# Kernel optimization log

Measured on AMD Instinct MI355X. Metric: run time of the kernel, lower is better.

Reference implementation:

```python
import jax, jax.numpy as jnp
import numpy as np
import math

N_EMBD = 1024
N_HEAD = 16
HEAD_DIM = N_EMBD // N_HEAD // 2  # 32
DEPTH = 1
LAMBDA_INIT = 0.8 - 0.6 * math.exp(-0.3 * (DEPTH - 1))  # 0.2
EPS = 1e-5


def setup_inputs() -> dict:
    key = jax.random.key(0)
    ks = jax.random.split(key, 8)
    B, T, C = 4, 1024, N_EMBD
    x = jax.random.normal(ks[0], (B, T, C), dtype=jnp.float32)
    w_attn = jax.random.normal(ks[1], (C, 3 * C), dtype=jnp.float32) * (1.0 / math.sqrt(C))
    w_proj = jax.random.normal(ks[2], (C, C), dtype=jnp.float32) * (1.0 / math.sqrt(C))
    lambda_q1 = jax.random.normal(ks[3], (HEAD_DIM,), dtype=jnp.float32) * 0.1
    lambda_q2 = jax.random.normal(ks[4], (HEAD_DIM,), dtype=jnp.float32) * 0.1
    lambda_k1 = jax.random.normal(ks[5], (HEAD_DIM,), dtype=jnp.float32) * 0.1
    lambda_k2 = jax.random.normal(ks[6], (HEAD_DIM,), dtype=jnp.float32) * 0.1
    gamma = jnp.ones((2 * HEAD_DIM,), dtype=jnp.float32)  # RMSNorm affine weight
    return {"x": x, "w_attn": w_attn, "w_proj": w_proj,
            "lambda_q1": lambda_q1, "lambda_q2": lambda_q2,
            "lambda_k1": lambda_k1, "lambda_k2": lambda_k2, "gamma": gamma}


def reference(x, w_attn, w_proj, lambda_q1, lambda_q2, lambda_k1, lambda_k2, gamma):
    B, T, C = x.shape
    H, hd = N_HEAD, HEAD_DIM
    qkv = x @ w_attn                                  # [B,T,3C]
    q, k, v = jnp.split(qkv, 3, axis=-1)
    q = q.reshape(B, T, 2 * H, hd).transpose(0, 2, 1, 3)   # [B,2H,T,hd]
    k = k.reshape(B, T, 2 * H, hd).transpose(0, 2, 1, 3)   # [B,2H,T,hd]
    v = v.reshape(B, T, H, 2 * hd).transpose(0, 2, 1, 3)   # [B,H,T,2hd]
    q = q * (hd ** -0.5)
    att = jnp.einsum('bhtd,bhsd->bhts', q, k) * (1.0 / math.sqrt(hd))
    causal = jnp.tril(jnp.ones((T, T), dtype=bool))
    att = jnp.where(causal, att, -jnp.inf)
    att = jax.nn.softmax(att, axis=-1)                # [B,2H,T,T]
    lam1 = jnp.exp(jnp.sum(lambda_q1 * lambda_k1))
    lam2 = jnp.exp(jnp.sum(lambda_q2 * lambda_k2))
    lambda_full = lam1 - lam2 + LAMBDA_INIT
    att = att.reshape(B, H, 2, T, T)
    att = att[:, :, 0] - lambda_full * att[:, :, 1]   # [B,H,T,T]
    out = jnp.einsum('bhts,bhsd->bhtd', att, v)       # [B,H,T,2hd]
    # RMSNorm over last dim with affine weight
    rms = jax.lax.rsqrt(jnp.mean(out * out, axis=-1, keepdims=True) + EPS)
    out = out * rms * gamma
    out = (1.0 - LAMBDA_INIT) * out
    out = out.transpose(0, 2, 1, 3).reshape(B, T, C)
    return out @ w_proj
```

## Files before the change

### kernel.cpp

```cpp
#include <hip/hip_runtime.h>

typedef unsigned short u16;
typedef unsigned int u32;
typedef __bf16 bf16x8 __attribute__((ext_vector_type(8)));
typedef float f32x4 __attribute__((ext_vector_type(4)));
typedef u16 u16x8 __attribute__((ext_vector_type(8)));
typedef u16 u16x4 __attribute__((ext_vector_type(4)));

#define DEV static __device__ __forceinline__

template <bool B> struct BC { static constexpr bool value = B; };

DEV u16 f2bf(float f) {
  unsigned u = __builtin_bit_cast(unsigned, f);
  u += 0x7fffu + ((u >> 16) & 1u);
  return (u16)(u >> 16);
}
DEV u16 f2bf_fast(float f) {
  unsigned u = __builtin_bit_cast(unsigned, f);
  return (u16)((u + 0x8000u) >> 16);
}
DEV float fexp2(float x) {
  float r;
  asm("v_exp_f32 %0, %1" : "=v"(r) : "v"(x));
  return r;
}

DEV void gld16(const void* g, void* l) {
  __builtin_amdgcn_global_load_lds((__attribute__((address_space(1))) void*)(g),
                                   (__attribute__((address_space(3))) void*)(l),
                                   16, 0, 0);
}

__global__ __launch_bounds__(256) void k_cast(const float* __restrict__ in,
                                              u16* __restrict__ out, int n4) {
  int i = blockIdx.x * 256 + threadIdx.x;
  if (i >= n4) return;
  float4 v = ((const float4*)in)[i];
  u16x4 r = { f2bf(v.x), f2bf(v.y), f2bf(v.z), f2bf(v.w) };
  ((u16x4*)out)[i] = r;
}

__global__ __launch_bounds__(256) void k_transpose_cast(const float* __restrict__ in,
                                                        u16* __restrict__ out,
                                                        int R, int Cc) {
  __shared__ u16 tile[64][65];
  int r0 = blockIdx.x * 64, c0 = blockIdx.y * 64;
  int tid = threadIdx.x;
#pragma unroll
  for (int rr = 0; rr < 4; ++rr) {
    int r = rr * 16 + (tid >> 4);
    int c = (tid & 15) * 4;
    float4 v = *(const float4*)&in[(size_t)(r0 + r) * Cc + c0 + c];
    tile[r][c + 0] = f2bf(v.x); tile[r][c + 1] = f2bf(v.y);
    tile[r][c + 2] = f2bf(v.z); tile[r][c + 3] = f2bf(v.w);
  }
  __syncthreads();
#pragma unroll
  for (int rr = 0; rr < 2; ++rr) {
    int cr = rr * 32 + (tid >> 3);
    int rc = (tid & 7) * 8;
    u16x8 v;
#pragma unroll
    for (int j = 0; j < 8; ++j) v[j] = tile[rc + j][cr];
    *(u16x8*)&out[(size_t)(c0 + cr) * R + r0 + rc] = v;
  }
}

__global__ __launch_bounds__(256) void k_vtrans(const u16* __restrict__ qkv,
                                                u16* __restrict__ vt) {
  __shared__ u16 tile[64][65];
  int bid = blockIdx.x;
  int b = bid >> 8, h = (bid >> 4) & 15, tt = bid & 15;
  int tid = threadIdx.x;
#pragma unroll
  for (int rr = 0; rr < 2; ++rr) {
    int tl = rr * 32 + (tid >> 3);
    int d0 = (tid & 7) * 8;
    u16x8 v = *(const u16x8*)&qkv[(size_t)(b * 1024 + tt * 64 + tl) * 3072 + 2048 + h * 64 + d0];
#pragma unroll
    for (int j = 0; j < 8; ++j) tile[tl][d0 + j] = v[j];
  }
  __syncthreads();
#pragma unroll
  for (int rr = 0; rr < 2; ++rr) {
    int d = rr * 32 + (tid >> 3);
    int t0 = (tid & 7) * 8;
    u16x8 v;
#pragma unroll
    for (int j = 0; j < 8; ++j) v[j] = tile[t0 + j][d];
    *(u16x8*)&vt[((size_t)(b * 16 + h) * 64 + d) * 1024 + tt * 64 + t0] = v;
  }
}

__global__ void k_lambda(const float* lq1, const float* lq2,
                         const float* lk1, const float* lk2, float* out) {
  int i = threadIdx.x;
  float a = 0.f, b = 0.f;
  if (i < 32) { a = lq1[i] * lk1[i]; b = lq2[i] * lk2[i]; }
#pragma unroll
  for (int s = 1; s < 64; s <<= 1) { a += __shfl_xor(a, s); b += __shfl_xor(b, s); }
  if (i == 0) out[0] = __expf(a) - __expf(b) + 0.2f;
}

template <bool OUT_F32>
__global__ __launch_bounds__(256) void k_gemm(const u16* __restrict__ A,
                                              const u16* __restrict__ Bt,
                                              void* __restrict__ Cout,
                                              int M, int N, int K) {
  __shared__ __align__(16) u16 As[3][128 * 32];
  __shared__ __align__(16) u16 Bs[3][128 * 32];
  int tid = threadIdx.x;
  int nbn = N >> 7;
  int wg = ((int)blockIdx.x & 7) * ((int)gridDim.x >> 3) + ((int)blockIdx.x >> 3);
  int bm = wg / nbn, bn = wg % nbn;
  int m0 = bm << 7, n0 = bn << 7;
  int lane = tid & 63, w = tid >> 6, wm = w >> 1, wn = w & 1;
  int lr = lane & 15, lg = lane >> 4;
  const u16* pA0; const u16* pA1; const u16* pB0; const u16* pB1;
  {
    int i0 = tid, i1 = tid + 256;
    int r0 = i0 >> 2, s80 = (i0 & 3) ^ ((r0 >> 1) & 3);
    int r1 = i1 >> 2, s81 = (i1 & 3) ^ ((r1 >> 1) & 3);
    pA0 = &A[(size_t)(m0 + r0) * K + s80 * 8];
    pA1 = &A[(size_t)(m0 + r1) * K + s81 * 8];
    pB0 = &Bt[(size_t)(n0 + r0) * K + s80 * 8];
    pB1 = &Bt[(size_t)(n0 + r1) * K + s81 * 8];
  }
  f32x4 acc[4][4] = {};
  auto stage = [&](int kt, int buf) {
    gld16(pA0 + kt, &As[buf][tid * 8]);
    gld16(pA1 + kt, &As[buf][(tid + 256) * 8]);
    gld16(pB0 + kt, &Bs[buf][tid * 8]);
    gld16(pB1 + kt, &Bs[buf][(tid + 256) * 8]);
  };
  int NK = K >> 5;
  stage(0, 0);
  if (NK > 1) stage(32, 1);
  for (int ki = 0; ki < NK; ++ki) {
    if (ki + 1 < NK) {
      asm volatile("s_waitcnt vmcnt(4)" ::: "memory");
    } else {
      asm volatile("s_waitcnt vmcnt(0)" ::: "memory");
    }
    __builtin_amdgcn_s_barrier();
    __builtin_amdgcn_sched_barrier(0);
    if (ki + 2 < NK) stage((ki + 2) << 5, (ki + 2) % 3);
    int cur = ki % 3;
    bf16x8 af[4], bfr[4];
#pragma unroll
    for (int m = 0; m < 4; ++m) {
      int r = wm * 64 + m * 16 + lr;
      int c8 = lg ^ ((r >> 1) & 3);
      af[m] = *(const bf16x8*)&As[cur][r * 32 + c8 * 8];
    }
#pragma unroll
    for (int n = 0; n < 4; ++n) {
      int r = wn * 64 + n * 16 + lr;
      int c8 = lg ^ ((r >> 1) & 3);
      bfr[n] = *(const bf16x8*)&Bs[cur][r * 32 + c8 * 8];
    }
    __builtin_amdgcn_s_setprio(1);
#pragma unroll
    for (int m = 0; m < 4; ++m)
#pragma unroll
      for (int n = 0; n < 4; ++n)
        acc[m][n] = __builtin_amdgcn_mfma_f32_16x16x32_bf16(af[m], bfr[n], acc[m][n], 0, 0, 0);
    __builtin_amdgcn_s_setprio(0);
    __builtin_amdgcn_sched_barrier(0);
  }
#pragma unroll
  for (int m = 0; m < 4; ++m)
#pragma unroll
    for (int r = 0; r < 4; ++r) {
      int gr = m0 + wm * 64 + m * 16 + lg * 4 + r;
#pragma unroll
      for (int n = 0; n < 4; ++n) {
        int gc = n0 + wn * 64 + n * 16 + lr;
        if (OUT_F32) ((float*)Cout)[(size_t)gr * N + gc] = acc[m][n][r];
        else ((u16*)Cout)[(size_t)gr * N + gc] = f2bf(acc[m][n][r]);
      }
    }
}

__global__ __launch_bounds__(256) void k_diffattn(const u16* __restrict__ qkv,
                                                  const u16* __restrict__ vt,
                                                  const float* __restrict__ lam_p,
                                                  const float* __restrict__ gamma,
                                                  u16* __restrict__ attn_out) {
  __shared__ __align__(16) u16 Ks[2][2][64 * 32];
  __shared__ __align__(16) u16 Vs[2][64 * 64];
  __shared__ __align__(16) u16 Ps[4][2][16 * 72];
  int bid = blockIdx.x;
  int qb = 15 - (bid >> 6);
  int b = (bid >> 4) & 3, h = bid & 15;
  int tid = threadIdx.x, lane = tid & 63, w = tid >> 6;
  int lr = lane & 15, lg = lane >> 4;
  int g1 = 2 * h, g2 = g1 + 1;
  float lam = *lam_p;
  const float cexp = 0.045084222f;
  f32x4 zero = {0.f, 0.f, 0.f, 0.f};
  u16* P1 = &Ps[w][0][0];
  u16* P2 = &Ps[w][1][0];

  const u16* pK1; const u16* pK2;
  {
    int r = tid >> 2, c8 = tid & 3;
    int s8 = c8 ^ ((r >> 1) & 3);
    size_t krow = (size_t)(b * 1024 + r) * 3072 + 1024;
    pK1 = qkv + krow + g1 * 32 + s8 * 8;
    pK2 = qkv + krow + g2 * 32 + s8 * 8;
  }
  const u16* pV0; const u16* pV1;
  {
    const u16* vbase = vt + ((size_t)(b * 16 + h) * 64) * 1024;
    int d0 = tid >> 3, o0 = (tid & 7) ^ (d0 & 7);
    pV0 = vbase + (size_t)d0 * 1024 + o0 * 8;
    pV1 = vbase + (size_t)(d0 + 32) * 1024 + o0 * 8;
  }

  auto stage = [&](int s0, int buf) {
    gld16(pK1 + (size_t)s0 * 3072, &Ks[buf][0][tid * 8]);
    gld16(pK2 + (size_t)s0 * 3072, &Ks[buf][1][tid * 8]);
    gld16(pV0 + s0, &Vs[buf][tid * 8]);
    gld16(pV1 + s0, &Vs[buf][(tid + 256) * 8]);
  };

  int q0 = qb * 64;
  size_t qrow = (size_t)(b * 1024 + q0 + w * 16 + lr);
  bf16x8 qf1 = *(const bf16x8*)&qkv[qrow * 3072 + g1 * 32 + lg * 8];
  bf16x8 qf2 = *(const bf16x8*)&qkv[qrow * 3072 + g2 * 32 + lg * 8];
  f32x4 o1[4] = {}, o2[4] = {};
  float l1[4] = {}, l2[4] = {};
  int qg_base = q0 + w * 16 + lg * 4;

  auto tile = [&](int cur, int s0, auto mk) {
    f32x4 s1[4], s2[4];
    __builtin_amdgcn_s_setprio(1);
#pragma unroll
    for (int ni = 0; ni < 4; ++ni) {
      int rk = ni * 16 + lr;
      int c8 = lg ^ ((rk >> 1) & 3);
      bf16x8 kf1 = *(const bf16x8*)&Ks[cur][0][rk * 32 + c8 * 8];
      bf16x8 kf2 = *(const bf16x8*)&Ks[cur][1][rk * 32 + c8 * 8];
      s1[ni] = __builtin_amdgcn_mfma_f32_16x16x32_bf16(qf1, kf1, zero, 0, 0, 0);
      s2[ni] = __builtin_amdgcn_mfma_f32_16x16x32_bf16(qf2, kf2, zero, 0, 0, 0);
    }
    __builtin_amdgcn_s_setprio(0);
#pragma unroll
    for (int ni = 0; ni < 4; ++ni) {
      int sg = s0 + ni * 16 + lr;
#pragma unroll
      for (int r = 0; r < 4; ++r) {
        float v1 = fexp2(s1[ni][r] * cexp);
        float v2 = fexp2(s2[ni][r] * cexp);
        if constexpr (decltype(mk)::value) {
          if (sg > qg_base + r) { v1 = 0.f; v2 = 0.f; }
        }
        l1[r] += v1; l2[r] += v2;
        P1[(lg * 4 + r) * 72 + ni * 16 + lr] = f2bf_fast(v1);
        P2[(lg * 4 + r) * 72 + ni * 16 + lr] = f2bf_fast(v2);
      }
    }
    __builtin_amdgcn_s_setprio(1);
#pragma unroll
    for (int kk = 0; kk < 2; ++kk) {
      bf16x8 pa1 = *(const bf16x8*)&P1[lr * 72 + kk * 32 + lg * 8];
      bf16x8 pa2 = *(const bf16x8*)&P2[lr * 72 + kk * 32 + lg * 8];
#pragma unroll
      for (int ni = 0; ni < 4; ++ni) {
        int d = ni * 16 + lr;
        int c8 = (kk * 4 + lg) ^ (d & 7);
        bf16x8 vb = *(const bf16x8*)&Vs[cur][d * 64 + c8 * 8];
        o1[ni] = __builtin_amdgcn_mfma_f32_16x16x32_bf16(pa1, vb, o1[ni], 0, 0, 0);
        o2[ni] = __builtin_amdgcn_mfma_f32_16x16x32_bf16(pa2, vb, o2[ni], 0, 0, 0);
      }
    }
    __builtin_amdgcn_s_setprio(0);
  };

  stage(0, 0);
  for (int t = 0; t < qb; ++t) {
    int cur = t & 1;
    stage((t + 1) * 64, cur ^ 1);
    asm volatile("s_waitcnt vmcnt(4)" ::: "memory");
    __builtin_amdgcn_s_barrier();
    __builtin_amdgcn_sched_barrier(0);
    tile(cur, t * 64, BC<false>{});
    __builtin_amdgcn_sched_barrier(0);
    __builtin_amdgcn_s_barrier();
  }
  asm volatile("s_waitcnt vmcnt(0)" ::: "memory");
  __builtin_amdgcn_s_barrier();
  __builtin_amdgcn_sched_barrier(0);
  tile(qb & 1, q0, BC<true>{});

#pragma unroll
  for (int r = 0; r < 4; ++r) {
    l1[r] += __shfl_xor(l1[r], 1); l1[r] += __shfl_xor(l1[r], 2);
    l1[r] += __shfl_xor(l1[r], 4); l1[r] += __shfl_xor(l1[r], 8);
    l2[r] += __shfl_xor(l2[r], 1); l2[r] += __shfl_xor(l2[r], 2);
    l2[r] += __shfl_xor(l2[r], 4); l2[r] += __shfl_xor(l2[r], 8);
  }
  float val[4][4];
#pragma unroll
  for (int ni = 0; ni < 4; ++ni)
#pragma unroll
    for (int r = 0; r < 4; ++r)
      val[ni][r] = o1[ni][r] * (1.f / l1[r]) - lam * (o2[ni][r] * (1.f / l2[r]));
#pragma unroll
  for (int r = 0; r < 4; ++r) {
    float ss = 0.f;
#pragma unroll
    for (int ni = 0; ni < 4; ++ni) ss += val[ni][r] * val[ni][r];
    ss += __shfl_xor(ss, 1); ss += __shfl_xor(ss, 2);
    ss += __shfl_xor(ss, 4); ss += __shfl_xor(ss, 8);
    float sc = rsqrtf(ss * (1.f / 64.f) + 1e-5f) * 0.8f;
#pragma unroll
    for (int ni = 0; ni < 4; ++ni) val[ni][r] *= sc;
  }
#pragma unroll
  for (int ni = 0; ni < 4; ++ni) {
    int d = ni * 16 + lr;
    float g = gamma[d];
#pragma unroll
    for (int r = 0; r < 4; ++r) {
      int trow = q0 + w * 16 + lg * 4 + r;
      attn_out[(size_t)(b * 1024 + trow) * 1024 + h * 64 + d] = f2bf(val[ni][r] * g);
    }
  }
}

extern "C" void kernel_launch(void* const* d_in, const int* in_sizes, int n_in,
                              void* d_out, int out_size, void* d_ws, size_t ws_size,
                              hipStream_t stream) {
  const float* x   = (const float*)d_in[0];
  const float* wa  = (const float*)d_in[1];
  const float* wp  = (const float*)d_in[2];
  const float* lq1 = (const float*)d_in[3];
  const float* lq2 = (const float*)d_in[4];
  const float* lk1 = (const float*)d_in[5];
  const float* lk2 = (const float*)d_in[6];
  const float* gam = (const float*)d_in[7];
  float* out = (float*)d_out;

  char* ws = (char*)d_ws;
  u16* xb   = (u16*)(ws);
  u16* wab  = (u16*)(ws + (8ull << 20));
  u16* wpb  = (u16*)(ws + (14ull << 20));
  u16* qkv  = (u16*)(ws + (16ull << 20));
  u16* vt   = (u16*)(ws + (40ull << 20));
  u16* aout = (u16*)(ws + (48ull << 20));
  float* lam = (float*)(ws + (56ull << 20));

  k_cast<<<4096, 256, 0, stream>>>(x, xb, 1024 * 1024);
  k_transpose_cast<<<dim3(16, 48), 256, 0, stream>>>(wa, wab, 1024, 3072);
  k_transpose_cast<<<dim3(16, 16), 256, 0, stream>>>(wp, wpb, 1024, 1024);
  k_lambda<<<1, 64, 0, stream>>>(lq1, lq2, lk1, lk2, lam);
  k_gemm<false><<<32 * 24, 256, 0, stream>>>(xb, wab, qkv, 4096, 3072, 1024);
  k_vtrans<<<1024, 256, 0, stream>>>(qkv, vt);
  k_diffattn<<<1024, 256, 0, stream>>>(qkv, vt, lam, gam, aout);
  k_gemm<true><<<32 * 8, 256, 0, stream>>>(aout, wpb, out, 4096, 1024, 1024);
}
```

Baseline: 186.3 us.

## Merge prep kernels into one launch and remap GEMM tiles per XCD

Folds the x cast, both weight transpose-casts and the lambda computation into a single k_prep kernel that branches on block index, cutting three kernel launches and the gaps between them. It also changes the GEMM block-to-tile mapping so that each XCD works on a contiguous rectangular region of the output (a quarter of the M blocks by half of the N blocks), aiming for better L2 reuse of A and B tiles within each XCD. The fused prep kernel is heterogeneous, so its blocks can be unevenly balanced, and the new mapping assumes nbm is divisible by 4 and nbn by 2.

Result: faster. 180.4 us (-3.2%).

```diff
diff --git a/kernel.cpp b/kernel.cpp
--- a/kernel.cpp
+++ b/kernel.cpp
@@ -32,21 +32,39 @@
                                    16, 0, 0);
 }
 
-__global__ __launch_bounds__(256) void k_cast(const float* __restrict__ in,
-                                              u16* __restrict__ out, int n4) {
-  int i = blockIdx.x * 256 + threadIdx.x;
-  if (i >= n4) return;
-  float4 v = ((const float4*)in)[i];
-  u16x4 r = { f2bf(v.x), f2bf(v.y), f2bf(v.z), f2bf(v.w) };
-  ((u16x4*)out)[i] = r;
-}
-
-__global__ __launch_bounds__(256) void k_transpose_cast(const float* __restrict__ in,
-                                                        u16* __restrict__ out,
-                                                        int R, int Cc) {
+__global__ __launch_bounds__(256) void k_prep(const float* __restrict__ x,
+                                              const float* __restrict__ wa,
+                                              const float* __restrict__ wp,
+                                              const float* __restrict__ lq1,
+                                              const float* __restrict__ lq2,
+                                              const float* __restrict__ lk1,
+                                              const float* __restrict__ lk2,
+                                              u16* __restrict__ xb,
+                                              u16* __restrict__ wab,
+                                              u16* __restrict__ wpb,
+                                              float* __restrict__ lam) {
   __shared__ u16 tile[64][65];
-  int r0 = blockIdx.x * 64, c0 = blockIdx.y * 64;
-  int tid = threadIdx.x;
+  int bid = blockIdx.x, tid = threadIdx.x;
+  if (bid < 4096) {
+    int i = bid * 256 + tid;
+    float4 v = ((const float4*)x)[i];
+    u16x4 r = { f2bf(v.x), f2bf(v.y), f2bf(v.z), f2bf(v.w) };
+    ((u16x4*)xb)[i] = r;
+    return;
+  }
+  if (bid == 5120) {
+    int i = tid;
+    float a = 0.f, b = 0.f;
+    if (i < 32) { a = lq1[i] * lk1[i]; b = lq2[i] * lk2[i]; }
+#pragma unroll
+    for (int s = 1; s < 64; s <<= 1) { a += __shfl_xor(a, s); b += __shfl_xor(b, s); }
+    if (i == 0) lam[0] = __expf(a) - __expf(b) + 0.2f;
+    return;
+  }
+  const float* in; u16* out; int R, Cc, local;
+  if (bid < 4864) { in = wa; out = wab; R = 1024; Cc = 3072; local = bid - 4096; }
+  else            { in = wp; out = wpb; R = 1024; Cc = 1024; local = bid - 4864; }
+  int r0 = (local & 15) * 64, c0 = (local >> 4) * 64;
 #pragma unroll
   for (int rr = 0; rr < 4; ++rr) {
     int r = rr * 16 + (tid >> 4);
@@ -91,16 +109,6 @@
     for (int j = 0; j < 8; ++j) v[j] = tile[t0 + j][d];
     *(u16x8*)&vt[((size_t)(b * 16 + h) * 64 + d) * 1024 + tt * 64 + t0] = v;
   }
-}
-
-__global__ void k_lambda(const float* lq1, const float* lq2,
-                         const float* lk1, const float* lk2, float* out) {
-  int i = threadIdx.x;
-  float a = 0.f, b = 0.f;
-  if (i < 32) { a = lq1[i] * lk1[i]; b = lq2[i] * lk2[i]; }
-#pragma unroll
-  for (int s = 1; s < 64; s <<= 1) { a += __shfl_xor(a, s); b += __shfl_xor(b, s); }
-  if (i == 0) out[0] = __expf(a) - __expf(b) + 0.2f;
 }
 
 template <bool OUT_F32>
@@ -111,9 +119,12 @@
   __shared__ __align__(16) u16 As[3][128 * 32];
   __shared__ __align__(16) u16 Bs[3][128 * 32];
   int tid = threadIdx.x;
-  int nbn = N >> 7;
-  int wg = ((int)blockIdx.x & 7) * ((int)gridDim.x >> 3) + ((int)blockIdx.x >> 3);
-  int bm = wg / nbn, bn = wg % nbn;
+  int nbm = M >> 7, nbn = N >> 7;
+  int xcd = (int)blockIdx.x & 7;
+  int local = (int)blockIdx.x >> 3;
+  int rm = nbm >> 2, rn = nbn >> 1;
+  int bm = (xcd >> 1) * rm + local % rm;
+  int bn = (xcd & 1) * rn + local / rm;
   int m0 = bm << 7, n0 = bn << 7;
   int lane = tid & 63, w = tid >> 6, wm = w >> 1, wn = w & 1;
   int lr = lane & 15, lg = lane >> 4;
@@ -353,10 +364,7 @@
   u16* aout = (u16*)(ws + (48ull << 20));
   float* lam = (float*)(ws + (56ull << 20));
 
-  k_cast<<<4096, 256, 0, stream>>>(x, xb, 1024 * 1024);
-  k_transpose_cast<<<dim3(16, 48), 256, 0, stream>>>(wa, wab, 1024, 3072);
-  k_transpose_cast<<<dim3(16, 16), 256, 0, stream>>>(wp, wpb, 1024, 1024);
-  k_lambda<<<1, 64, 0, stream>>>(lq1, lq2, lk1, lk2, lam);
+  k_prep<<<5121, 256, 0, stream>>>(x, wa, wp, lq1, lq2, lk1, lk2, xb, wab, wpb, lam);
   k_gemm<false><<<32 * 24, 256, 0, stream>>>(xb, wab, qkv, 4096, 3072, 1024);
   k_vtrans<<<1024, 256, 0, stream>>>(qkv, vt);
   k_diffattn<<<1024, 256, 0, stream>>>(qkv, vt, lam, gam, aout);
```
